# Kernel optimization log

Hardware: AMD Instinct MI355X
Metric: run time of the kernel (lower is better)

Reference implementation:

```python
import jax, jax.numpy as jnp
import numpy as np

B, T, D, A = 32, 2048, 1024, 128


def setup_inputs() -> dict:
    key = jax.random.key(0)
    k1, k2, k3, k4 = jax.random.split(key, 4)
    x = jax.random.normal(k1, (B, T, D), dtype=jnp.float32)
    Ws = jax.random.normal(k2, (D, A), dtype=jnp.float32) * (1.0 / np.sqrt(D))
    bs = jax.random.normal(k3, (A,), dtype=jnp.float32) * 0.01
    us = jax.random.normal(k4, (A,), dtype=jnp.float32) * (1.0 / np.sqrt(A))
    return {"x": x, "Ws": Ws, "bs": bs, "us": us}


def reference(x, Ws, bs, us):
    # ui = tanh(x @ Ws + bs): [B, T, A]
    ui = jnp.tanh(jnp.einsum("btd,da->bta", x, Ws) + bs)
    # scalar score per timestep: [B, T]
    scores = jnp.einsum("bta,a->bt", ui, us)
    # exp / sum normalization over time == softmax over axis 1
    ai = jax.nn.softmax(scores, axis=1)
    # weighted sum over time: [B, D]
    return jnp.einsum("bt,btd->bd", ai, x)
```

## Files before the change

### kernel.cpp

```cpp
#include <hip/hip_runtime.h>
#include <hip/hip_bf16.h>

#define B_ 32
#define T_ 2048
#define D_ 1024
#define A_ 128

typedef __attribute__((ext_vector_type(8))) short bf16x8;
typedef __attribute__((ext_vector_type(4))) float f32x4;

static __device__ __forceinline__ unsigned short f2bf(float f) {
  union { float f; unsigned u; } v; v.f = f;
  unsigned r = v.u + 0x7FFFu + ((v.u >> 16) & 1u);
  return (unsigned short)(r >> 16);
}

static __device__ __forceinline__ unsigned cvt2u(float lo, float hi) {
  __hip_bfloat162 h2 = __float22bfloat162_rn(make_float2(lo, hi));
  unsigned u;
  __builtin_memcpy(&u, &h2, 4);
  return u;
}

static __device__ __forceinline__ void barrier_lds() {
  asm volatile("s_waitcnt lgkmcnt(0)\n\ts_barrier" ::: "memory");
}

__global__ __launch_bounds__(256) void k_prep(const float* __restrict__ Ws,
                                              unsigned short* __restrict__ Wt) {
  int i = blockIdx.x * 256 + threadIdx.x;
  int a = i >> 10, d = i & 1023;
  Wt[i] = f2bf(Ws[(size_t)d * A_ + a]);
}

#define LDRF 1028
#define LDRB 1032

__global__ __launch_bounds__(512, 2) void k_fused(const float* __restrict__ x,
                                                  const unsigned short* __restrict__ Wt,
                                                  const float* __restrict__ bs,
                                                  const float* __restrict__ us,
                                                  float* __restrict__ part,
                                                  float* __restrict__ Zp) {
  __shared__ __align__(16) float xb[16 * LDRF];
  __shared__ __align__(16) unsigned short ab[16 * LDRB];
  __shared__ float sc_part[16 * 8];
  __shared__ float e_lds[16];

  const int tid  = threadIdx.x;
  const int w    = tid >> 6;
  const int lane = tid & 63;
  const int lrow = lane & 15;
  const int g    = lane >> 4;
  const int sub  = blockIdx.x;
  const int b    = blockIdx.y;

  const int a_col = w * 16 + lrow;
  bf16x8 wreg[32];
  {
    const unsigned short* wr = Wt + (size_t)a_col * D_ + g * 8;
#pragma unroll
    for (int kt = 0; kt < 32; ++kt) wreg[kt] = *(const bf16x8*)(wr + kt * 32);
  }
  const float bsv = bs[a_col];
  const float usv = us[a_col];

  const int srow = w * 2 + (lane >> 5);
  const int scol = (lane & 31) * 4;
  const float* gx = x + ((size_t)b * T_ + (size_t)sub * 256) * D_;

  float4 st[8];
#pragma unroll
  for (int q = 0; q < 8; ++q)
    st[q] = *(const float4*)(gx + (size_t)srow * D_ + scol + q * 128);
#pragma unroll
  for (int q = 0; q < 8; ++q) {
    *(float4*)(&xb[srow * LDRF + scol + q * 128]) = st[q];
    unsigned lo = cvt2u(st[q].x, st[q].y);
    unsigned hi = cvt2u(st[q].z, st[q].w);
    *(uint2*)(&ab[srow * LDRB + scol + q * 128]) = make_uint2(lo, hi);
  }
  __syncthreads();

  float a0 = 0.f, a1 = 0.f, zacc = 0.f;

  for (int i = 0; i < 16; ++i) {
    if (i < 15) {
      const float* gc = gx + (size_t)(i + 1) * 16 * D_;
#pragma unroll
      for (int q = 0; q < 8; ++q)
        st[q] = *(const float4*)(gc + (size_t)srow * D_ + scol + q * 128);
    }
    __builtin_amdgcn_sched_barrier(0);

    f32x4 accm = (f32x4)0.f;
    const unsigned short* arow = ab + lrow * LDRB + g * 8;
#pragma unroll
    for (int kt = 0; kt < 32; ++kt) {
      bf16x8 af = *(const bf16x8*)(arow + kt * 32);
      accm = __builtin_amdgcn_mfma_f32_16x16x32_bf16(af, wreg[kt], accm, 0, 0, 0);
    }

#pragma unroll
    for (int r = 0; r < 4; ++r) {
      float p = usv * tanhf(accm[r] + bsv);
#pragma unroll
      for (int o = 1; o < 16; o <<= 1) p += __shfl_xor(p, o, 64);
      if (lrow == 0) sc_part[(g * 4 + r) * 8 + w] = p;
    }
    barrier_lds();

    if (tid < 16) {
      float s = 0.f;
#pragma unroll
      for (int ww = 0; ww < 8; ++ww) s += sc_part[tid * 8 + ww];
      e_lds[tid] = expf(s);
    }
    barrier_lds();

    const float* xd = xb + tid * 2;
#pragma unroll
    for (int t = 0; t < 16; ++t) {
      const float2 v = *(const float2*)(xd + t * LDRF);
      const float ev = e_lds[t];
      a0 = fmaf(ev, v.x, a0);
      a1 = fmaf(ev, v.y, a1);
      zacc += ev;
    }
    __syncthreads();

    if (i < 15) {
#pragma unroll
      for (int q = 0; q < 8; ++q) {
        *(float4*)(&xb[srow * LDRF + scol + q * 128]) = st[q];
        unsigned lo = cvt2u(st[q].x, st[q].y);
        unsigned hi = cvt2u(st[q].z, st[q].w);
        *(uint2*)(&ab[srow * LDRB + scol + q * 128]) = make_uint2(lo, hi);
      }
      __syncthreads();
    }
  }

  float* pp = part + ((size_t)sub * B_ + b) * D_ + tid * 2;
  *(float2*)pp = make_float2(a0, a1);
  if (tid == 0) Zp[b * 8 + sub] = zacc;
}

__global__ __launch_bounds__(256) void k_reduce(const float* __restrict__ part,
                                                const float* __restrict__ Zp,
                                                float* __restrict__ out) {
  const int i = blockIdx.x * 256 + threadIdx.x;
  const int b = i >> 10, d = i & 1023;
  float zs = 0.f;
#pragma unroll
  for (int s = 0; s < 8; ++s) zs += Zp[b * 8 + s];
  float acc = 0.f;
#pragma unroll
  for (int s = 0; s < 8; ++s) acc += part[((size_t)s * B_ + b) * D_ + d];
  out[i] = acc / zs;
}

extern "C" void kernel_launch(void* const* d_in, const int* in_sizes, int n_in,
                              void* d_out, int out_size, void* d_ws, size_t ws_size,
                              hipStream_t stream) {
  const float* x  = (const float*)d_in[0];
  const float* Ws = (const float*)d_in[1];
  const float* bs = (const float*)d_in[2];
  const float* us = (const float*)d_in[3];
  float* out = (float*)d_out;

  char* ws = (char*)d_ws;
  unsigned short* Wt = (unsigned short*)ws;
  float* part = (float*)(ws + (256 << 10));
  float* Zp   = (float*)(ws + (256 << 10) + (1 << 20));

  k_prep<<<512, 256, 0, stream>>>(Ws, Wt);
  k_fused<<<dim3(8, B_), 512, 0, stream>>>(x, Wt, bs, us, part, Zp);
  k_reduce<<<(B_ * D_) / 256, 256, 0, stream>>>(part, Zp, out);
}
```

Baseline: 73.35 us.

## Keep x tiles in registers, double-buffer loads, drop fp32 LDS staging

The fused kernel no longer stages fp32 x in LDS. Each thread keeps its loaded x slice in registers, ping-pongs two register buffers so the next chunk's global load overlaps the MFMA scoring, and accumulates e·x directly into per-row register accumulators, reduced across the 16 rows through LDS once at the end. Each thread now computes exp of its own row score, which removes the extra barrier and the single-thread e_lds stage. This cuts LDS traffic and barriers per chunk, but register pressure rises sharply (wreg plus two 8×float4 buffers plus 8 accumulators) under launch_bounds(512,2), which risks spills.

```diff
diff --git a/kernel.cpp b/kernel.cpp
--- a/kernel.cpp
+++ b/kernel.cpp
@@ -33,8 +33,8 @@
   Wt[i] = f2bf(Ws[(size_t)d * A_ + a]);
 }
 
+#define LDRB 1032
 #define LDRF 1028
-#define LDRB 1032
 
 __global__ __launch_bounds__(512, 2) void k_fused(const float* __restrict__ x,
                                                   const unsigned short* __restrict__ Wt,
@@ -42,10 +42,10 @@
                                                   const float* __restrict__ us,
                                                   float* __restrict__ part,
                                                   float* __restrict__ Zp) {
-  __shared__ __align__(16) float xb[16 * LDRF];
-  __shared__ __align__(16) unsigned short ab[16 * LDRB];
+  __shared__ __align__(16) char smem[16 * LDRF * 4];
   __shared__ float sc_part[16 * 8];
-  __shared__ float e_lds[16];
+  unsigned short* ab = (unsigned short*)smem;
+  float* red = (float*)smem;
 
   const int tid  = threadIdx.x;
   const int w    = tid >> 6;
@@ -66,84 +66,121 @@
   const float usv = us[a_col];
 
   const int srow = w * 2 + (lane >> 5);
-  const int scol = (lane & 31) * 4;
+  const int scol = (lane & 31) * 8;
   const float* gx = x + ((size_t)b * T_ + (size_t)sub * 256) * D_;
 
-  float4 st[8];
-#pragma unroll
-  for (int q = 0; q < 8; ++q)
-    st[q] = *(const float4*)(gx + (size_t)srow * D_ + scol + q * 128);
-#pragma unroll
-  for (int q = 0; q < 8; ++q) {
-    *(float4*)(&xb[srow * LDRF + scol + q * 128]) = st[q];
-    unsigned lo = cvt2u(st[q].x, st[q].y);
-    unsigned hi = cvt2u(st[q].z, st[q].w);
-    *(uint2*)(&ab[srow * LDRB + scol + q * 128]) = make_uint2(lo, hi);
-  }
-  __syncthreads();
-
-  float a0 = 0.f, a1 = 0.f, zacc = 0.f;
-
-  for (int i = 0; i < 16; ++i) {
-    if (i < 15) {
-      const float* gc = gx + (size_t)(i + 1) * 16 * D_;
-#pragma unroll
-      for (int q = 0; q < 8; ++q)
-        st[q] = *(const float4*)(gc + (size_t)srow * D_ + scol + q * 128);
+#define ISSUE(dst, ci)                                                            \
+  {                                                                               \
+    const float* gp_ = gx + (size_t)(ci) * 16 * D_ + (size_t)srow * D_ + scol;    \
+    _Pragma("unroll") for (int q = 0; q < 4; ++q) {                               \
+      dst[2 * q]     = *(const float4*)(gp_ + q * 256);                           \
+      dst[2 * q + 1] = *(const float4*)(gp_ + q * 256 + 4);                       \
+    }                                                                             \
+  }
+
+#define WRITE_AB(src)                                                             \
+  {                                                                               \
+    _Pragma("unroll") for (int q = 0; q < 4; ++q) {                               \
+      uint4 h_;                                                                   \
+      h_.x = cvt2u(src[2 * q].x, src[2 * q].y);                                   \
+      h_.y = cvt2u(src[2 * q].z, src[2 * q].w);                                   \
+      h_.z = cvt2u(src[2 * q + 1].x, src[2 * q + 1].y);                           \
+      h_.w = cvt2u(src[2 * q + 1].z, src[2 * q + 1].w);                           \
+      *(uint4*)(&ab[srow * LDRB + scol + q * 256]) = h_;                          \
+    }                                                                             \
+  }
+
+#define SCORE_TO_E(e_out)                                                         \
+  {                                                                               \
+    f32x4 accm = (f32x4)0.f;                                                      \
+    const unsigned short* arow = ab + lrow * LDRB + g * 8;                        \
+    _Pragma("unroll") for (int kt = 0; kt < 32; ++kt) {                           \
+      bf16x8 af = *(const bf16x8*)(arow + kt * 32);                               \
+      accm = __builtin_amdgcn_mfma_f32_16x16x32_bf16(af, wreg[kt], accm, 0, 0, 0);\
+    }                                                                             \
+    _Pragma("unroll") for (int r = 0; r < 4; ++r) {                               \
+      float p = usv * tanhf(accm[r] + bsv);                                       \
+      _Pragma("unroll") for (int o = 1; o < 16; o <<= 1) p += __shfl_xor(p, o, 64);\
+      if (lrow == 0) sc_part[(g * 4 + r) * 8 + w] = p;                            \
+    }                                                                             \
+    barrier_lds();                                                                \
+    const float4 p0 = *(const float4*)(sc_part + srow * 8);                       \
+    const float4 p1 = *(const float4*)(sc_part + srow * 8 + 4);                   \
+    e_out = expf(p0.x + p0.y + p0.z + p0.w + p1.x + p1.y + p1.z + p1.w);          \
+  }
+
+  float4 stA[8], stB[8];
+  f32x4 acc[8];
+#pragma unroll
+  for (int j = 0; j < 8; ++j) acc[j] = (f32x4)0.f;
+  float zacc = 0.f;
+
+  ISSUE(stA, 0);
+  ISSUE(stB, 1);
+  __builtin_amdgcn_sched_barrier(0);
+  WRITE_AB(stA);
+  barrier_lds();
+
+  for (int i = 0; i < 16; i += 2) {
+    {
+      float e;
+      SCORE_TO_E(e);
+      zacc += e;
+#pragma unroll
+      for (int j = 0; j < 8; ++j) {
+        acc[j][0] = fmaf(e, stA[j].x, acc[j][0]);
+        acc[j][1] = fmaf(e, stA[j].y, acc[j][1]);
+        acc[j][2] = fmaf(e, stA[j].z, acc[j][2]);
+        acc[j][3] = fmaf(e, stA[j].w, acc[j][3]);
+      }
+      if (i < 14) ISSUE(stA, i + 2);
+      __builtin_amdgcn_sched_barrier(0);
+      WRITE_AB(stB);
+      barrier_lds();
     }
-    __builtin_amdgcn_sched_barrier(0);
-
-    f32x4 accm = (f32x4)0.f;
-    const unsigned short* arow = ab + lrow * LDRB + g * 8;
-#pragma unroll
-    for (int kt = 0; kt < 32; ++kt) {
-      bf16x8 af = *(const bf16x8*)(arow + kt * 32);
-      accm = __builtin_amdgcn_mfma_f32_16x16x32_bf16(af, wreg[kt], accm, 0, 0, 0);
+    {
+      float e;
+      SCORE_TO_E(e);
+      zacc += e;
+#pragma unroll
+      for (int j = 0; j < 8; ++j) {
+        acc[j][0] = fmaf(e, stB[j].x, acc[j][0]);
+        acc[j][1] = fmaf(e, stB[j].y, acc[j][1]);
+        acc[j][2] = fmaf(e, stB[j].z, acc[j][2]);
+        acc[j][3] = fmaf(e, stB[j].w, acc[j][3]);
+      }
+      if (i + 3 < 16) ISSUE(stB, i + 3);
+      __builtin_amdgcn_sched_barrier(0);
+      if (i < 14) WRITE_AB(stA);
+      barrier_lds();
     }
-
-#pragma unroll
-    for (int r = 0; r < 4; ++r) {
-      float p = usv * tanhf(accm[r] + bsv);
-#pragma unroll
-      for (int o = 1; o < 16; o <<= 1) p += __shfl_xor(p, o, 64);
-      if (lrow == 0) sc_part[(g * 4 + r) * 8 + w] = p;
-    }
-    barrier_lds();
-
-    if (tid < 16) {
-      float s = 0.f;
-#pragma unroll
-      for (int ww = 0; ww < 8; ++ww) s += sc_part[tid * 8 + ww];
-      e_lds[tid] = expf(s);
-    }
-    barrier_lds();
-
-    const float* xd = xb + tid * 2;
-#pragma unroll
-    for (int t = 0; t < 16; ++t) {
-      const float2 v = *(const float2*)(xd + t * LDRF);
-      const float ev = e_lds[t];
-      a0 = fmaf(ev, v.x, a0);
-      a1 = fmaf(ev, v.y, a1);
-      zacc += ev;
-    }
-    __syncthreads();
-
-    if (i < 15) {
-#pragma unroll
-      for (int q = 0; q < 8; ++q) {
-        *(float4*)(&xb[srow * LDRF + scol + q * 128]) = st[q];
-        unsigned lo = cvt2u(st[q].x, st[q].y);
-        unsigned hi = cvt2u(st[q].z, st[q].w);
-        *(uint2*)(&ab[srow * LDRB + scol + q * 128]) = make_uint2(lo, hi);
-      }
-      __syncthreads();
-    }
-  }
-
-  float* pp = part + ((size_t)sub * B_ + b) * D_ + tid * 2;
-  *(float2*)pp = make_float2(a0, a1);
-  if (tid == 0) Zp[b * 8 + sub] = zacc;
+  }
+
+  if ((lane & 31) == 0) sc_part[srow] = zacc;
+#pragma unroll
+  for (int q = 0; q < 4; ++q) {
+    *(f32x4*)(&red[srow * LDRF + scol + q * 256])     = acc[2 * q];
+    *(f32x4*)(&red[srow * LDRF + scol + q * 256 + 4]) = acc[2 * q + 1];
+  }
+  barrier_lds();
+
+  float s0 = 0.f, s1 = 0.f;
+#pragma unroll
+  for (int r = 0; r < 16; ++r) {
+    const float2 v = *(const float2*)(&red[r * LDRF + tid * 2]);
+    s0 += v.x;
+    s1 += v.y;
+  }
+  *(float2*)(part + ((size_t)sub * B_ + b) * D_ + tid * 2) = make_float2(s0, s1);
+  if (tid == 0) {
+    float Z = 0.f;
+#pragma unroll
+    for (int r = 0; r < 16; ++r) Z += sc_part[r];
+    Zp[b * 8 + sub] = Z;
+  }
+#undef ISSUE
+#undef WRITE_AB
+#undef SCORE_TO_E
 }
 
 __global__ __launch_bounds__(256) void k_reduce(const float* __restrict__ part,
```

Measured after the change: 172.0 us. 2.35x slower.
